# Kernel tuning notes

Hardware: AMD Instinct MI355X
Metric: run time of the kernel (lower is better)

Reference implementation:

```python
import jax, jax.numpy as jnp
import numpy as np
import math

N, T, D_MODEL = 4, 2048, 1024
NHEAD = 16
HEAD_DIM = D_MODEL // NHEAD
ROTARY_DIM = 64
WINDOW = (128, 128)
ROPE_BASE = 10000.0


def _rope_cos_sin(seq_len, rotary_dim, dtype):
    # non-interleaved (GPT-NeoX style) rotary embedding tables
    inv_freq = 1.0 / (ROPE_BASE ** (jnp.arange(0, rotary_dim, 2, dtype=jnp.float32) / rotary_dim))
    t = jnp.arange(seq_len, dtype=jnp.float32)
    freqs = jnp.outer(t, inv_freq)  # [T, rotary_dim//2]
    return jnp.cos(freqs).astype(dtype), jnp.sin(freqs).astype(dtype)


def _apply_rope(x, cos, sin):
    # x: [N, T, H, D]; rotate first ROTARY_DIM dims, pass the rest through
    r = ROTARY_DIM
    x_rot, x_pass = x[..., :r], x[..., r:]
    x1, x2 = x_rot[..., : r // 2], x_rot[..., r // 2 :]
    c = cos[None, :, None, :]
    s = sin[None, :, None, :]
    out = jnp.concatenate([x1 * c - x2 * s, x1 * s + x2 * c], axis=-1)
    return jnp.concatenate([out, x_pass], axis=-1)


def _sliding_window_bias(seq_len, window, dtype):
    i = jnp.arange(seq_len)[:, None]
    j = jnp.arange(seq_len)[None, :]
    # triu(diag=-w0) & tril(diag=w1): keep j - i in [-w0, w1]
    keep = (j - i >= -window[0]) & (j - i <= window[1])
    return jnp.where(keep, jnp.zeros((), dtype), jnp.full((), -jnp.inf, dtype))


def setup_inputs() -> dict:
    key = jax.random.key(0)
    k1, k2, k3 = jax.random.split(key, 3)
    x = jax.random.normal(k1, (N, T, D_MODEL), dtype=jnp.float32)
    Wqkv = jax.random.normal(k2, (D_MODEL, 3 * D_MODEL), dtype=jnp.float32) * (1.0 / math.sqrt(D_MODEL))
    Wout = jax.random.normal(k3, (D_MODEL, D_MODEL), dtype=jnp.float32) * (1.0 / math.sqrt(D_MODEL))
    bout = jnp.zeros((D_MODEL,), dtype=jnp.float32)
    return {"x": x, "Wqkv": Wqkv, "Wout": Wout, "bout": bout}


def reference(x, Wqkv, Wout, bout):
    n, t, _ = x.shape
    qkv = (x @ Wqkv).reshape(n, t, 3, NHEAD, HEAD_DIM)
    q, k, v = qkv[:, :, 0], qkv[:, :, 1], qkv[:, :, 2]  # each [N, T, H, D]
    cos, sin = _rope_cos_sin(t, ROTARY_DIM, x.dtype)
    q = _apply_rope(q, cos, sin)
    k = _apply_rope(k, cos, sin)
    scale = 1.0 / math.sqrt(HEAD_DIM)
    bias = _sliding_window_bias(t, WINDOW, x.dtype)  # [T, T]
    scores = jnp.einsum("bthd,bshd->bhts", q, k) * scale + bias[None, None]
    attn = jax.nn.softmax(scores, axis=-1)
    out = jnp.einsum("bhts,bshd->bthd", attn, v).reshape(n, t, D_MODEL)
    return out @ Wout + bout
```

## Files before the change

kernel.cpp:

```cpp
#include <hip/hip_runtime.h>
#include <hip/hip_bf16.h>
#include <cstdint>
#include <cstddef>

typedef __bf16 bf16_t;
typedef bf16_t bf16x8 __attribute__((ext_vector_type(8)));
typedef float f32x4 __attribute__((ext_vector_type(4)));
typedef unsigned short ushort_t;

#define T_SEQ 2048
#define DM 1024
#define NH 16
#define HD 64
#define WIN 128
#define ROPE_C 0.28782313662425572f
#define SCALE_LOG2E 0.18033688011112042f
#define ATT_M 16.0f

__device__ __forceinline__ ushort_t f2bf(float f) {
    union { float f; unsigned u; } v; v.f = f;
    unsigned r = v.u + 0x7fff + ((v.u >> 16) & 1);
    return (ushort_t)(r >> 16);
}
__device__ __forceinline__ float sane(float v, float sent) {
    return (fabsf(v) < 1e30f) ? v : sent;
}
__device__ __forceinline__ void gld16(const ushort_t* g, ushort_t* l) {
    __builtin_amdgcn_global_load_lds(
        (const __attribute__((address_space(1))) unsigned int*)g,
        (__attribute__((address_space(3))) unsigned int*)l, 16, 0, 0);
}

__global__ __launch_bounds__(256) void kzero_f(float* __restrict__ p) {
    size_t i = ((size_t)blockIdx.x * 256 + threadIdx.x) * 4;
    float4 z; z.x = z.y = z.z = z.w = 0.f;
    *(float4*)(p + i) = z;
}

__device__ __forceinline__ void trans_f2b_tile(const float* __restrict__ in,
                                               ushort_t* __restrict__ out,
                                               int R, int C, int c0, int r0) {
    __shared__ __align__(16) ushort_t tile[64][72];
    const int tid = threadIdx.x;
    const int rl = tid >> 2, q4 = tid & 3;
    const float* src = in + (size_t)(r0 + rl) * C + c0 + q4 * 16;
    ushort_t cv[16];
#pragma unroll
    for (int i = 0; i < 4; i++) {
        float4 f = *(const float4*)(src + i * 4);
        cv[i * 4 + 0] = f2bf(f.x); cv[i * 4 + 1] = f2bf(f.y);
        cv[i * 4 + 2] = f2bf(f.z); cv[i * 4 + 3] = f2bf(f.w);
    }
    *(uint4*)&tile[rl][q4 * 16]     = *(uint4*)&cv[0];
    *(uint4*)&tile[rl][q4 * 16 + 8] = *(uint4*)&cv[8];
    __syncthreads();
    const int cl = tid >> 2;
    ushort_t tmp[16];
#pragma unroll
    for (int i = 0; i < 16; i++) tmp[i] = tile[q4 * 16 + i][cl];
    ushort_t* dst = out + (size_t)(c0 + cl) * R + r0 + q4 * 16;
    *(uint4*)(dst)     = *(uint4*)&tmp[0];
    *(uint4*)(dst + 8) = *(uint4*)&tmp[8];
}

__global__ __launch_bounds__(256) void prep(const float* __restrict__ x,
                                            const float* __restrict__ Wqkv,
                                            const float* __restrict__ Wout,
                                            ushort_t* __restrict__ xb,
                                            ushort_t* __restrict__ WqkvT,
                                            ushort_t* __restrict__ WoutT) {
    const int bx = blockIdx.x;
    if (bx < 4096) {
        size_t i = ((size_t)bx * 256 + threadIdx.x) * 8;
        float4 a0 = *(const float4*)(x + i);
        float4 a1 = *(const float4*)(x + i + 4);
        ushort_t cv[8];
        cv[0] = f2bf(a0.x); cv[1] = f2bf(a0.y); cv[2] = f2bf(a0.z); cv[3] = f2bf(a0.w);
        cv[4] = f2bf(a1.x); cv[5] = f2bf(a1.y); cv[6] = f2bf(a1.z); cv[7] = f2bf(a1.w);
        *(uint4*)(xb + i) = *(uint4*)cv;
    } else if (bx < 4864) {
        int tb = bx - 4096;
        trans_f2b_tile(Wqkv, WqkvT, 1024, 3072, (tb % 48) * 64, (tb / 48) * 64);
    } else {
        int tb = bx - 4864;
        trans_f2b_tile(Wout, WoutT, 1024, 1024, (tb & 15) * 64, (tb >> 4) * 64);
    }
}

#define BM 128
#define BN 256
#define BK 32
#define KTILES 32
#define LBUF ((BM + BN) * BK)
#define LTOT (3 * LBUF)

__device__ __forceinline__ void gemm_core(const ushort_t* __restrict__ Agl,
                                          const ushort_t* __restrict__ Bgl,
                                          ushort_t* L, int m0, int n0,
                                          f32x4 (&acc)[8][4]) {
    const int tid = threadIdx.x;
    const int lane = tid & 63, w = tid >> 6;
    const int c = lane & 15, g = lane >> 4;
    const int sv   = (lane & 7) ^ (lane >> 3);
    const int grow = 2 * (lane >> 3) + (sv >> 2);
    const int gcol = (sv & 3) * 8;
    const int loff = (c >> 1) * 64 + (((((c & 1) << 2) | g) ^ ((c >> 1) & 7)) * 8);

#pragma unroll
    for (int mi = 0; mi < 8; ++mi)
#pragma unroll
        for (int ni = 0; ni < 4; ++ni)
#pragma unroll
            for (int r = 0; r < 4; ++r) acc[mi][ni][r] = 0.f;

    auto STAGE = [&](int kt, int bo) {
        const int k0 = kt * BK;
#pragma unroll
        for (int j = 0; j < 2; ++j) {
            const ushort_t* ga = Agl + (size_t)(m0 + 32 * w + 16 * j + grow) * 1024 + k0 + gcol;
            gld16(ga, &L[bo + (w * 2 + j) * 512]);
        }
#pragma unroll
        for (int j = 0; j < 4; ++j) {
            const ushort_t* gb = Bgl + (size_t)(n0 + 64 * w + 16 * j + grow) * 1024 + k0 + gcol;
            gld16(gb, &L[bo + BM * BK + (w * 4 + j) * 512]);
        }
    };

    STAGE(0, 0);
    STAGE(1, LBUF);
    asm volatile("s_waitcnt vmcnt(6)\n\ts_barrier" ::: "memory");

    int bcur = 0;
    for (int kt = 0; kt < KTILES; ++kt) {
        int bst = bcur + 2 * LBUF; if (bst >= LTOT) bst -= LTOT;
        if (kt + 2 < KTILES) STAGE(kt + 2, bst);

        const ushort_t* La = L + bcur;
        const ushort_t* Bb = La + BM * BK;
        bf16x8 bfr[4], af0[4], af1[4];
#pragma unroll
        for (int ni = 0; ni < 4; ++ni)
            bfr[ni] = *(const bf16x8*)&Bb[w * 2048 + ni * 512 + loff];
#pragma unroll
        for (int mi = 0; mi < 4; ++mi)
            af0[mi] = *(const bf16x8*)&La[mi * 512 + loff];
        __builtin_amdgcn_s_setprio(1);
#pragma unroll
        for (int mi = 0; mi < 4; ++mi)
#pragma unroll
            for (int ni = 0; ni < 4; ++ni)
                acc[mi][ni] = __builtin_amdgcn_mfma_f32_16x16x32_bf16(
                    af0[mi], bfr[ni], acc[mi][ni], 0, 0, 0);
        __builtin_amdgcn_s_setprio(0);
#pragma unroll
        for (int mi = 0; mi < 4; ++mi)
            af1[mi] = *(const bf16x8*)&La[(mi + 4) * 512 + loff];
        __builtin_amdgcn_s_setprio(1);
#pragma unroll
        for (int mi = 0; mi < 4; ++mi)
#pragma unroll
            for (int ni = 0; ni < 4; ++ni)
                acc[mi + 4][ni] = __builtin_amdgcn_mfma_f32_16x16x32_bf16(
                    af1[mi], bfr[ni], acc[mi + 4][ni], 0, 0, 0);
        __builtin_amdgcn_s_setprio(0);
        if (kt < KTILES - 2)
            asm volatile("s_waitcnt vmcnt(6)\n\ts_barrier" ::: "memory");
        else if (kt == KTILES - 2)
            asm volatile("s_waitcnt vmcnt(0)\n\ts_barrier" ::: "memory");
        bcur += LBUF; if (bcur == LTOT) bcur = 0;
    }
}

__global__ __launch_bounds__(256, 2) void gemm_qkv(const ushort_t* __restrict__ A,
                                                   const ushort_t* __restrict__ Bt,
                                                   ushort_t* __restrict__ Qr,
                                                   ushort_t* __restrict__ Kr,
                                                   ushort_t* __restrict__ Vt) {
    __shared__ __align__(16) ushort_t L[LTOT];
    const int m0 = blockIdx.x * BM, n0 = blockIdx.y * BN;
    f32x4 acc[8][4];
    gemm_core(A, Bt, L, m0, n0, acc);

    const int lane = threadIdx.x & 63, w = threadIdx.x >> 6;
    const int c = lane & 15, g = lane >> 4;
    const int nb = n0 + w * 64;
    const int sec = nb >> 10;
    const int h = (nb >> 6) & 15;

    if (sec < 2) {
        ushort_t* dst = (sec == 0) ? Qr : Kr;
        const float invf0 = __expf(-(float)(c) * ROPE_C);
        const float invf1 = __expf(-(float)(16 + c) * ROPE_C);
#pragma unroll
        for (int mi = 0; mi < 8; ++mi)
#pragma unroll
            for (int r = 0; r < 4; ++r) {
                int tg = m0 + mi * 16 + g * 4 + r;
                int nB = tg >> 11, t = tg & (T_SEQ - 1);
                float a0 = (float)t * invf0, a1 = (float)t * invf1;
                float s0 = __sinf(a0), c0 = __cosf(a0);
                float s1 = __sinf(a1), c1 = __cosf(a1);
                size_t base = ((size_t)(nB * NH + h) * T_SEQ + t) * 64;
                float x1a = acc[mi][0][r], x2a = acc[mi][2][r];
                float x1b = acc[mi][1][r], x2b = acc[mi][3][r];
                dst[base + c]      = f2bf(sane(x1a * c0 - x2a * s0, 1e3f));
                dst[base + 16 + c] = f2bf(sane(x1b * c1 - x2b * s1, 1e3f));
                dst[base + 32 + c] = f2bf(sane(x1a * s0 + x2a * c0, 1e3f));
                dst[base + 48 + c] = f2bf(sane(x1b * s1 + x2b * c1, 1e3f));
            }
    } else {
#pragma unroll
        for (int mi = 0; mi < 8; ++mi) {
            int tgb = m0 + mi * 16 + g * 4;
            int nB = tgb >> 11, t = tgb & (T_SEQ - 1);
            size_t vrow = (size_t)(nB * NH + h) * 64 * T_SEQ;
#pragma unroll
            for (int ni = 0; ni < 4; ++ni) {
                ushort4 pk;
                pk.x = f2bf(sane(acc[mi][ni][0], 1e3f));
                pk.y = f2bf(sane(acc[mi][ni][1], 1e3f));
                pk.z = f2bf(sane(acc[mi][ni][2], 1e3f));
                pk.w = f2bf(sane(acc[mi][ni][3], 1e3f));
                *(ushort4*)&Vt[vrow + (size_t)(ni * 16 + c) * T_SEQ + t] = pk;
            }
        }
    }
}

__global__ __launch_bounds__(256, 2) void gemm_out(const ushort_t* __restrict__ A,
                                                   const ushort_t* __restrict__ Bt,
                                                   float* __restrict__ C,
                                                   const float* __restrict__ bias) {
    __shared__ __align__(16) ushort_t L[LTOT];
    const int m0 = blockIdx.x * BM, n0 = blockIdx.y * BN;
    f32x4 acc[8][4];
    gemm_core(A, Bt, L, m0, n0, acc);

    const int lane = threadIdx.x & 63, w = threadIdx.x >> 6;
    const int c = lane & 15, g = lane >> 4;
#pragma unroll
    for (int ni = 0; ni < 4; ++ni) {
        int col = n0 + w * 64 + ni * 16 + c;
        float bv = bias[col];
#pragma unroll
        for (int mi = 0; mi < 8; ++mi)
#pragma unroll
            for (int r = 0; r < 4; ++r) {
                int rowi = m0 + mi * 16 + g * 4 + r;
                C[(size_t)rowi * 1024 + col] = sane(acc[mi][ni][r] + bv, 1e8f);
            }
    }
}

__global__ __launch_bounds__(256) void attn_swin(const ushort_t* __restrict__ Qr,
                                                 const ushort_t* __restrict__ Kr,
                                                 const ushort_t* __restrict__ Vt,
                                                 ushort_t* __restrict__ O) {
    __shared__ __align__(16) ushort_t pbuf[4][2][16 * 32];
    const int tid = threadIdx.x;
    const int wid = tid >> 6, lane = tid & 63;
    const int qb = (blockIdx.x & 15) * 128;
    const int h = (blockIdx.x >> 4) & 15, n = blockIdx.x >> 8;
    const int c = lane & 15, g = lane >> 4;
    const size_t hb = ((size_t)(n * NH + h)) * T_SEQ * 64;
    const int t0s[2] = { qb + wid * 16, qb + 64 + wid * 16 };

    bf16x8 qf0[2], qf1[2];
#pragma unroll
    for (int sub = 0; sub < 2; sub++) {
        qf0[sub] = *(const bf16x8*)(Qr + hb + (size_t)(t0s[sub] + c) * 64 + g * 8);
        qf1[sub] = *(const bf16x8*)(Qr + hb + (size_t)(t0s[sub] + c) * 64 + 32 + g * 8);
    }

    f32x4 o[2][4];
    float l_r[2][4];
#pragma unroll
    for (int sub = 0; sub < 2; sub++)
#pragma unroll
        for (int i = 0; i < 4; i++) {
            l_r[sub][i] = 0.f;
#pragma unroll
            for (int r = 0; r < 4; r++) o[sub][i][r] = 0.f;
        }

    int sB_lo = qb - WIN;        if (sB_lo < 0) sB_lo = 0;
    int sB_hi = qb + 127 + WIN;  if (sB_hi > T_SEQ - 1) sB_hi = T_SEQ - 1;

    for (int s0 = sB_lo; s0 <= sB_hi; s0 += 32) {
        bool act[2];
#pragma unroll
        for (int sub = 0; sub < 2; sub++)
            act[sub] = !(s0 > t0s[sub] + 143 || s0 + 31 < t0s[sub] - WIN);
        if (!act[0] && !act[1]) continue;

#pragma unroll
        for (int sub = 0; sub < 2; sub++) {
            if (!act[sub]) continue;
            const int t0 = t0s[sub];
            f32x4 S[2];
#pragma unroll
            for (int sh = 0; sh < 2; sh++) {
                const ushort_t* kb = Kr + hb + (size_t)(s0 + sh * 16 + c) * 64;
                bf16x8 kf0 = *(const bf16x8*)(kb + g * 8);
                bf16x8 kf1 = *(const bf16x8*)(kb + 32 + g * 8);
                f32x4 z;
#pragma unroll
                for (int r = 0; r < 4; r++) z[r] = 0.f;
                z = __builtin_amdgcn_mfma_f32_16x16x32_bf16(qf0[sub], kf0, z, 0, 0, 0);
                z = __builtin_amdgcn_mfma_f32_16x16x32_bf16(qf1[sub], kf1, z, 0, 0, 0);
                S[sh] = z;
            }
            const bool interior = (s0 >= t0 - 113) && (s0 <= t0 + 97);
            ushort_t* pb = pbuf[wid][sub];
            if (interior) {
#pragma unroll
                for (int sh = 0; sh < 2; sh++)
#pragma unroll
                    for (int r = 0; r < 4; r++) {
                        float p = exp2f(S[sh][r] * SCALE_LOG2E - ATT_M);
                        l_r[sub][r] += p;
                        pb[(g * 4 + r) * 32 + sh * 16 + c] = f2bf(p);
                    }
            } else {
#pragma unroll
                for (int sh = 0; sh < 2; sh++)
#pragma unroll
                    for (int r = 0; r < 4; r++) {
                        int s = s0 + sh * 16 + c;
                        int q = t0 + g * 4 + r;
                        bool keep = (s - q >= -WIN) && (s - q <= WIN);
                        float v = keep ? S[sh][r] * SCALE_LOG2E : -1e30f;
                        float p = exp2f(v - ATT_M);
                        l_r[sub][r] += p;
                        pb[(g * 4 + r) * 32 + sh * 16 + c] = f2bf(p);
                    }
            }
        }
        __asm__ volatile("s_waitcnt lgkmcnt(0)" ::: "memory");
#pragma unroll
        for (int sub = 0; sub < 2; sub++) {
            if (!act[sub]) continue;
            bf16x8 pf = *(const bf16x8*)&pbuf[wid][sub][c * 32 + g * 8];
#pragma unroll
            for (int di = 0; di < 4; di++) {
                bf16x8 vf = *(const bf16x8*)(Vt + hb +
                                (size_t)(di * 16 + c) * T_SEQ + s0 + g * 8);
                o[sub][di] = __builtin_amdgcn_mfma_f32_16x16x32_bf16(pf, vf, o[sub][di], 0, 0, 0);
            }
        }
        __asm__ volatile("" ::: "memory");
    }

#pragma unroll
    for (int sub = 0; sub < 2; sub++) {
#pragma unroll
        for (int off = 1; off < 16; off <<= 1)
#pragma unroll
            for (int r = 0; r < 4; r++)
                l_r[sub][r] += __shfl_xor(l_r[sub][r], off, 64);
        float inv[4];
#pragma unroll
        for (int r = 0; r < 4; r++) inv[r] = __builtin_amdgcn_rcpf(l_r[sub][r]);
#pragma unroll
        for (int di = 0; di < 4; di++)
#pragma unroll
            for (int r = 0; r < 4; r++) {
                int q = t0s[sub] + g * 4 + r;
                float val = o[sub][di][r] * inv[r];
                O[((size_t)(n * T_SEQ + q)) * DM + h * 64 + di * 16 + c] =
                    f2bf(sane(val, 1e6f));
            }
    }
}

extern "C" void kernel_launch(void* const* d_in, const int* in_sizes, int n_in,
                              void* d_out, int out_size, void* d_ws, size_t ws_size,
                              hipStream_t stream) {
    const float* x    = (const float*)d_in[0];
    const float* Wqkv = (const float*)d_in[1];
    const float* Wout = (const float*)d_in[2];
    const float* bout = (const float*)d_in[3];
    float* out = (float*)d_out;

    const size_t NEED = 72ull << 20;
    if (ws_size < NEED) {
        kzero_f<<<dim3(8192), 256, 0, stream>>>(out);
        return;
    }
    char* ws = (char*)d_ws;
    ushort_t* WqkvT = (ushort_t*)(ws);
    ushort_t* WoutT = (ushort_t*)(ws + (6ull << 20));
    ushort_t* Qr    = (ushort_t*)(ws + (8ull << 20));
    ushort_t* Kr    = (ushort_t*)(ws + (24ull << 20));
    ushort_t* Vt    = (ushort_t*)(ws + (40ull << 20));
    ushort_t* xb    = (ushort_t*)(ws + (56ull << 20));
    ushort_t* Oat   = xb;

    prep<<<dim3(5120), 256, 0, stream>>>(x, Wqkv, Wout, xb, WqkvT, WoutT);
    gemm_qkv<<<dim3(64, 12), 256, 0, stream>>>(xb, WqkvT, Qr, Kr, Vt);
    attn_swin<<<dim3(1024), 256, 0, stream>>>(Qr, Kr, Vt, Oat);
    gemm_out<<<dim3(64, 4), 256, 0, stream>>>(Oat, WoutT, out, bout);
}
```

Before: 245.0 us.

## Stage K/V tiles in LDS for attention and remap GEMM blocks across XCDs

The attention kernel now loads 64-row K and V tiles cooperatively into padded shared memory, prefetching the next tile into registers. All four waves then reuse those tiles instead of each wave reading K and V directly from global memory in 32-column steps, which cuts redundant global traffic and doubles the work per iteration. Separately, both GEMMs switch to a 1D grid with a block-id swizzle ((id&7)*stride + id>>3), so consecutive blocks land on the same XCD and share L2. The trade-off is extra barriers and LDS use per block, and the tile loop only prefetches when a full 64-row tile fits inside the window range.

Result: faster. 219.1 us (-10.6%).

```diff
diff --git a/kernel.cpp b/kernel.cpp
--- a/kernel.cpp
+++ b/kernel.cpp
@@ -154,7 +154,7 @@
                     af0[mi], bfr[ni], acc[mi][ni], 0, 0, 0);
         __builtin_amdgcn_s_setprio(0);
 #pragma unroll
-        for (int mi = 0; mi < 4; ++mi)
+    for (int mi = 0; mi < 4; ++mi)
             af1[mi] = *(const bf16x8*)&La[(mi + 4) * 512 + loff];
         __builtin_amdgcn_s_setprio(1);
 #pragma unroll
@@ -178,7 +178,9 @@
                                                    ushort_t* __restrict__ Kr,
                                                    ushort_t* __restrict__ Vt) {
     __shared__ __align__(16) ushort_t L[LTOT];
-    const int m0 = blockIdx.x * BM, n0 = blockIdx.y * BN;
+    const int id  = blockIdx.x;
+    const int nid = (id & 7) * 96 + (id >> 3);
+    const int m0 = (nid & 63) * BM, n0 = (nid >> 6) * BN;
     f32x4 acc[8][4];
     gemm_core(A, Bt, L, m0, n0, acc);
 
@@ -233,7 +235,9 @@
                                                    float* __restrict__ C,
                                                    const float* __restrict__ bias) {
     __shared__ __align__(16) ushort_t L[LTOT];
-    const int m0 = blockIdx.x * BM, n0 = blockIdx.y * BN;
+    const int id  = blockIdx.x;
+    const int nid = (id & 7) * 32 + (id >> 3);
+    const int m0 = (nid & 63) * BM, n0 = (nid >> 6) * BN;
     f32x4 acc[8][4];
     gemm_core(A, Bt, L, m0, n0, acc);
 
@@ -252,12 +256,16 @@
             }
     }
 }
+
+#define KVB 64
 
 __global__ __launch_bounds__(256) void attn_swin(const ushort_t* __restrict__ Qr,
                                                  const ushort_t* __restrict__ Kr,
                                                  const ushort_t* __restrict__ Vt,
                                                  ushort_t* __restrict__ O) {
-    __shared__ __align__(16) ushort_t pbuf[4][2][16 * 32];
+    __shared__ __align__(16) ushort_t Ks[KVB * 72];
+    __shared__ __align__(16) ushort_t Vs[64 * 72];
+    __shared__ __align__(16) ushort_t pbuf[4][2][16 * 72];
     const int tid = threadIdx.x;
     const int wid = tid >> 6, lane = tid & 63;
     const int qb = (blockIdx.x & 15) * 128;
@@ -265,6 +273,7 @@
     const int c = lane & 15, g = lane >> 4;
     const size_t hb = ((size_t)(n * NH + h)) * T_SEQ * 64;
     const int t0s[2] = { qb + wid * 16, qb + 64 + wid * 16 };
+    const int st_row = tid >> 2, st_col = (tid & 3) * 16;
 
     bf16x8 qf0[2], qf1[2];
 #pragma unroll
@@ -287,44 +296,72 @@
     int sB_lo = qb - WIN;        if (sB_lo < 0) sB_lo = 0;
     int sB_hi = qb + 127 + WIN;  if (sB_hi > T_SEQ - 1) sB_hi = T_SEQ - 1;
 
-    for (int s0 = sB_lo; s0 <= sB_hi; s0 += 32) {
+    uint4 kreg0 = *(const uint4*)(Kr + hb + (size_t)(sB_lo + st_row) * 64 + st_col);
+    uint4 kreg1 = *(const uint4*)(Kr + hb + (size_t)(sB_lo + st_row) * 64 + st_col + 8);
+    uint4 vreg0 = *(const uint4*)(Vt + hb + (size_t)st_row * T_SEQ + sB_lo + st_col);
+    uint4 vreg1 = *(const uint4*)(Vt + hb + (size_t)st_row * T_SEQ + sB_lo + st_col + 8);
+
+    for (int s0 = sB_lo; s0 <= sB_hi; s0 += KVB) {
+        __syncthreads();
+        *(uint4*)&Ks[st_row * 72 + st_col]     = kreg0;
+        *(uint4*)&Ks[st_row * 72 + st_col + 8] = kreg1;
+        *(uint4*)&Vs[st_row * 72 + st_col]     = vreg0;
+        *(uint4*)&Vs[st_row * 72 + st_col + 8] = vreg1;
+        __syncthreads();
+        int s1 = s0 + KVB;
+        if (s1 + KVB - 1 <= sB_hi) {
+            kreg0 = *(const uint4*)(Kr + hb + (size_t)(s1 + st_row) * 64 + st_col);
+            kreg1 = *(const uint4*)(Kr + hb + (size_t)(s1 + st_row) * 64 + st_col + 8);
+            vreg0 = *(const uint4*)(Vt + hb + (size_t)st_row * T_SEQ + s1 + st_col);
+            vreg1 = *(const uint4*)(Vt + hb + (size_t)st_row * T_SEQ + s1 + st_col + 8);
+        }
         bool act[2];
 #pragma unroll
         for (int sub = 0; sub < 2; sub++)
-            act[sub] = !(s0 > t0s[sub] + 143 || s0 + 31 < t0s[sub] - WIN);
+            act[sub] = !(s0 > t0s[sub] + 15 + WIN || s0 + KVB - 1 < t0s[sub] - WIN);
         if (!act[0] && !act[1]) continue;
+
+        bf16x8 kf0[4], kf1[4];
+#pragma unroll
+        for (int sh = 0; sh < 4; sh++) {
+            kf0[sh] = *(const bf16x8*)&Ks[(sh * 16 + c) * 72 + g * 8];
+            kf1[sh] = *(const bf16x8*)&Ks[(sh * 16 + c) * 72 + 32 + g * 8];
+        }
+        bf16x8 vfl[4], vfh[4];
+#pragma unroll
+        for (int di = 0; di < 4; di++) {
+            vfl[di] = *(const bf16x8*)&Vs[(di * 16 + c) * 72 + g * 8];
+            vfh[di] = *(const bf16x8*)&Vs[(di * 16 + c) * 72 + 32 + g * 8];
+        }
 
 #pragma unroll
         for (int sub = 0; sub < 2; sub++) {
             if (!act[sub]) continue;
             const int t0 = t0s[sub];
-            f32x4 S[2];
-#pragma unroll
-            for (int sh = 0; sh < 2; sh++) {
-                const ushort_t* kb = Kr + hb + (size_t)(s0 + sh * 16 + c) * 64;
-                bf16x8 kf0 = *(const bf16x8*)(kb + g * 8);
-                bf16x8 kf1 = *(const bf16x8*)(kb + 32 + g * 8);
+            f32x4 S[4];
+#pragma unroll
+            for (int sh = 0; sh < 4; sh++) {
                 f32x4 z;
 #pragma unroll
                 for (int r = 0; r < 4; r++) z[r] = 0.f;
-                z = __builtin_amdgcn_mfma_f32_16x16x32_bf16(qf0[sub], kf0, z, 0, 0, 0);
-                z = __builtin_amdgcn_mfma_f32_16x16x32_bf16(qf1[sub], kf1, z, 0, 0, 0);
+                z = __builtin_amdgcn_mfma_f32_16x16x32_bf16(qf0[sub], kf0[sh], z, 0, 0, 0);
+                z = __builtin_amdgcn_mfma_f32_16x16x32_bf16(qf1[sub], kf1[sh], z, 0, 0, 0);
                 S[sh] = z;
             }
-            const bool interior = (s0 >= t0 - 113) && (s0 <= t0 + 97);
+            const bool interior = (s0 >= t0 - 113) && (s0 <= t0 + 65);
             ushort_t* pb = pbuf[wid][sub];
             if (interior) {
 #pragma unroll
-                for (int sh = 0; sh < 2; sh++)
+                for (int sh = 0; sh < 4; sh++)
 #pragma unroll
                     for (int r = 0; r < 4; r++) {
                         float p = exp2f(S[sh][r] * SCALE_LOG2E - ATT_M);
                         l_r[sub][r] += p;
-                        pb[(g * 4 + r) * 32 + sh * 16 + c] = f2bf(p);
+                        pb[(g * 4 + r) * 72 + sh * 16 + c] = f2bf(p);
                     }
             } else {
 #pragma unroll
-                for (int sh = 0; sh < 2; sh++)
+                for (int sh = 0; sh < 4; sh++)
 #pragma unroll
                     for (int r = 0; r < 4; r++) {
                         int s = s0 + sh * 16 + c;
@@ -333,7 +370,7 @@
                         float v = keep ? S[sh][r] * SCALE_LOG2E : -1e30f;
                         float p = exp2f(v - ATT_M);
                         l_r[sub][r] += p;
-                        pb[(g * 4 + r) * 32 + sh * 16 + c] = f2bf(p);
+                        pb[(g * 4 + r) * 72 + sh * 16 + c] = f2bf(p);
                     }
             }
         }
@@ -341,12 +378,12 @@
 #pragma unroll
         for (int sub = 0; sub < 2; sub++) {
             if (!act[sub]) continue;
-            bf16x8 pf = *(const bf16x8*)&pbuf[wid][sub][c * 32 + g * 8];
+            bf16x8 pfl = *(const bf16x8*)&pbuf[wid][sub][c * 72 + g * 8];
+            bf16x8 pfh = *(const bf16x8*)&pbuf[wid][sub][c * 72 + 32 + g * 8];
 #pragma unroll
             for (int di = 0; di < 4; di++) {
-                bf16x8 vf = *(const bf16x8*)(Vt + hb +
-                                (size_t)(di * 16 + c) * T_SEQ + s0 + g * 8);
-                o[sub][di] = __builtin_amdgcn_mfma_f32_16x16x32_bf16(pf, vf, o[sub][di], 0, 0, 0);
+                o[sub][di] = __builtin_amdgcn_mfma_f32_16x16x32_bf16(pfl, vfl[di], o[sub][di], 0, 0, 0);
+                o[sub][di] = __builtin_amdgcn_mfma_f32_16x16x32_bf16(pfh, vfh[di], o[sub][di], 0, 0, 0);
             }
         }
         __asm__ volatile("" ::: "memory");
@@ -398,7 +435,7 @@
     ushort_t* Oat   = xb;
 
     prep<<<dim3(5120), 256, 0, stream>>>(x, Wqkv, Wout, xb, WqkvT, WoutT);
-    gemm_qkv<<<dim3(64, 12), 256, 0, stream>>>(xb, WqkvT, Qr, Kr, Vt);
+    gemm_qkv<<<dim3(768), 256, 0, stream>>>(xb, WqkvT, Qr, Kr, Vt);
     attn_swin<<<dim3(1024), 256, 0, stream>>>(Qr, Kr, Vt, Oat);
-    gemm_out<<<dim3(64, 4), 256, 0, stream>>>(Oat, WoutT, out, bout);
-}
+    gemm_out<<<dim3(256), 256, 0, stream>>>(Oat, WoutT, out, bout);
+}
```
